# Kernel optimization log

Hardware: AMD Instinct MI355X
Metric: run time of the kernel (lower is better)

Reference implementation:

```python
import jax, jax.numpy as jnp
import numpy as np


def setup_inputs() -> dict:
    key = jax.random.key(0)
    k1, k2 = jax.random.split(key)
    B, N, D = 32, 8192, 128
    queries = jax.random.normal(k1, (B, 1, D), dtype=jnp.float32)
    values = jax.random.normal(k2, (B, N, D), dtype=jnp.float32)
    return {"queries": queries, "values": values}


def reference(queries, values):
    # scores: bmm(q [B,1,D], v^T [B,D,N]) -> [B,1,N] -> squeeze -> [B,N]
    scores = jnp.einsum("bqd,bnd->bn", queries, values)
    attn = jax.nn.softmax(scores, axis=-1)            # [B, N]
    # weighted sum over N; no explicit repeat needed (broadcast instead)
    context = jnp.einsum("bn,bnd->bd", attn, values)  # [B, D]
    return (attn, context)
```

## Files before the change

kernel.cpp:

```cpp
#include <hip/hip_runtime.h>
#include <hip/hip_bf16.h>
#include <math.h>

#define B 32
#define NROWS 8192
#define D 128
#define CHUNK 256
#define NCHUNK (NROWS / CHUNK)
#define RPW (CHUNK / 4)
#define NIT (RPW / 4)
#define SHIFT 16.0f

template <int CTRL>
__device__ __forceinline__ float dpp_add(float x) {
    int y = __builtin_amdgcn_update_dpp(
        0, __float_as_int(x), CTRL, 0xf, 0xf, true);
    return x + __int_as_float(y);
}

__device__ __forceinline__ void half_reduce(float p, float& s_lo, float& s_hi) {
    p = dpp_add<0x111>(p);
    p = dpp_add<0x112>(p);
    p = dpp_add<0x114>(p);
    p = dpp_add<0x118>(p);
    p = dpp_add<0x142>(p);
    s_lo = __int_as_float(__builtin_amdgcn_readlane(__float_as_int(p), 31));
    s_hi = __int_as_float(__builtin_amdgcn_readlane(__float_as_int(p), 63));
}

__global__ __launch_bounds__(256) void attend_k1(
    const float* __restrict__ q,
    const float* __restrict__ v,
    float* __restrict__ out_scores,
    float* __restrict__ part_l,
    float* __restrict__ part_o)
{
    __shared__ float s_sc[CHUNK];
    __shared__ float wl4[4];
    __shared__ float wo[4][D];

    const int b    = blockIdx.x >> 5;
    const int c    = blockIdx.x & (NCHUNK - 1);
    const int n0   = c * CHUNK;
    const int tid  = threadIdx.x;
    const int w    = tid >> 6;
    const int lane = tid & 63;
    const int half = lane >> 5;
    const int l32  = lane & 31;

    const float4 q4 = ((const float4*)(q + b * D))[l32];
    const float4* vb = (const float4*)(v + ((size_t)b * NROWS + n0 + w * RPW) * D);

    float l = 0.f;
    float4 acc = make_float4(0.f, 0.f, 0.f, 0.f);

    float4 a0 = vb[lane];
    float4 a1 = vb[64 + lane];

    #pragma unroll 2
    for (int i = 0; i < NIT; ++i) {
        const int j = (i + 1 < NIT) ? i + 1 : i;
        const float4 b0 = vb[j * 128 + lane];
        const float4 b1 = vb[j * 128 + 64 + lane];

        float p0 = a0.x * q4.x + a0.y * q4.y + a0.z * q4.z + a0.w * q4.w;
        float p1 = a1.x * q4.x + a1.y * q4.y + a1.z * q4.z + a1.w * q4.w;

        float s0lo, s0hi, s1lo, s1hi;
        half_reduce(p0, s0lo, s0hi);
        half_reduce(p1, s1lo, s1hi);
        const float s0 = half ? s0hi : s0lo;
        const float s1 = half ? s1hi : s1lo;
        if (l32 == 0) {
            s_sc[w * RPW + 4 * i + half]     = s0;
            s_sc[w * RPW + 4 * i + 2 + half] = s1;
        }

        const float e0 = __expf(s0 - SHIFT);
        const float e1 = __expf(s1 - SHIFT);
        l += e0 + e1;
        acc.x += e0 * a0.x + e1 * a1.x;
        acc.y += e0 * a0.y + e1 * a1.y;
        acc.z += e0 * a0.z + e1 * a1.z;
        acc.w += e0 * a0.w + e1 * a1.w;

        a0 = b0; a1 = b1;
    }

    l += __shfl_xor(l, 32, 64);
    acc.x += __shfl_xor(acc.x, 32, 64);
    acc.y += __shfl_xor(acc.y, 32, 64);
    acc.z += __shfl_xor(acc.z, 32, 64);
    acc.w += __shfl_xor(acc.w, 32, 64);
    if (half == 0) {
        ((float4*)wo[w])[l32] = acc;
        if (l32 == 0) wl4[w] = l;
    }
    __syncthreads();

    out_scores[(size_t)b * NROWS + n0 + tid] = s_sc[tid];

    if (tid < D) {
        const float o = wo[0][tid] + wo[1][tid] + wo[2][tid] + wo[3][tid];
        part_o[(size_t)blockIdx.x * D + tid] = o;
        if (tid == 0)
            part_l[blockIdx.x] = wl4[0] + wl4[1] + wl4[2] + wl4[3];
    }
}

__global__ __launch_bounds__(128) void attend_k2(
    const float* __restrict__ part_l,
    const float* __restrict__ part_o,
    float* __restrict__ out_ctx,
    float* __restrict__ bInvL)
{
    const int b = blockIdx.x;
    const int d = threadIdx.x;

    float L = 0.f, o = 0.f;
    #pragma unroll
    for (int c = 0; c < NCHUNK; ++c) {
        L += part_l[b * NCHUNK + c];
        o += part_o[(size_t)(b * NCHUNK + c) * D + d];
    }
    out_ctx[b * D + d] = o / L;
    if (d == 0) bInvL[b] = 1.0f / L;
}

__global__ __launch_bounds__(256) void attend_k3(
    float* __restrict__ attn,
    const float* __restrict__ bInvL)
{
    const int idx = blockIdx.x * 256 + threadIdx.x;
    const int b   = idx >> 11;
    const float invL = bInvL[b];
    float4 s = ((float4*)attn)[idx];
    s.x = __expf(s.x - SHIFT) * invL;
    s.y = __expf(s.y - SHIFT) * invL;
    s.z = __expf(s.z - SHIFT) * invL;
    s.w = __expf(s.w - SHIFT) * invL;
    ((float4*)attn)[idx] = s;
}

extern "C" void kernel_launch(void* const* d_in, const int* in_sizes, int n_in,
                              void* d_out, int out_size, void* d_ws, size_t ws_size,
                              hipStream_t stream) {
    const float* q = (const float*)d_in[0];
    const float* v = (const float*)d_in[1];
    float* out = (float*)d_out;

    float* ws      = (float*)d_ws;
    float* part_l  = ws;
    float* part_o  = part_l + B * NCHUNK;
    float* bInvL   = part_o + (size_t)B * NCHUNK * D;

    attend_k1<<<B * NCHUNK, 256, 0, stream>>>(q, v, out, part_l, part_o);
    attend_k2<<<B, 128, 0, stream>>>(part_l, part_o, out + (size_t)B * NROWS, bInvL);
    attend_k3<<<(B * NROWS / 4) / 256, 256, 0, stream>>>(out, bInvL);
}
```

Baseline: 194.5 us.

## Fuse reduction and normalization into main kernel via last-block atomic counter

Merges the three kernels into one: each chunk block increments a per-batch atomic counter, and the last block for a batch combines the partial sums, writes the context, and normalizes that batch's attention row in place. This removes two kernel launches and their gaps, plus the separate pass over the attention output. In exchange it adds a memset launch and fence/atomic overhead, and leaves the normalization tail on just 32 blocks (one per batch), each looping over 8192 elements.

Result: slower. 324.0 us (+66.6%).

```diff
diff --git a/kernel.cpp b/kernel.cpp
--- a/kernel.cpp
+++ b/kernel.cpp
@@ -28,16 +28,18 @@
     s_hi = __int_as_float(__builtin_amdgcn_readlane(__float_as_int(p), 63));
 }
 
-__global__ __launch_bounds__(256) void attend_k1(
+__global__ __launch_bounds__(256) void attend_fused(
     const float* __restrict__ q,
     const float* __restrict__ v,
-    float* __restrict__ out_scores,
+    float* __restrict__ out,
     float* __restrict__ part_l,
-    float* __restrict__ part_o)
+    float* __restrict__ part_o,
+    int*   __restrict__ counters)
 {
     __shared__ float s_sc[CHUNK];
     __shared__ float wl4[4];
     __shared__ float wo[4][D];
+    __shared__ int   sh_last;
 
     const int b    = blockIdx.x >> 5;
     const int c    = blockIdx.x & (NCHUNK - 1);
@@ -98,7 +100,7 @@
     }
     __syncthreads();
 
-    out_scores[(size_t)b * NROWS + n0 + tid] = s_sc[tid];
+    out[(size_t)b * NROWS + n0 + tid] = s_sc[tid];
 
     if (tid < D) {
         const float o = wo[0][tid] + wo[1][tid] + wo[2][tid] + wo[3][tid];
@@ -106,40 +108,40 @@
         if (tid == 0)
             part_l[blockIdx.x] = wl4[0] + wl4[1] + wl4[2] + wl4[3];
     }
-}
 
-__global__ __launch_bounds__(128) void attend_k2(
-    const float* __restrict__ part_l,
-    const float* __restrict__ part_o,
-    float* __restrict__ out_ctx,
-    float* __restrict__ bInvL)
-{
-    const int b = blockIdx.x;
-    const int d = threadIdx.x;
+    __threadfence();
+    __syncthreads();
+    if (tid == 0)
+        sh_last = (atomicAdd(&counters[b], 1) == NCHUNK - 1);
+    __syncthreads();
+    if (!sh_last) return;
 
-    float L = 0.f, o = 0.f;
+    __threadfence();
+
+    float L = 0.f;
     #pragma unroll
-    for (int c = 0; c < NCHUNK; ++c) {
-        L += part_l[b * NCHUNK + c];
-        o += part_o[(size_t)(b * NCHUNK + c) * D + d];
+    for (int cc = 0; cc < NCHUNK; ++cc)
+        L += part_l[b * NCHUNK + cc];
+    const float invL = 1.0f / L;
+
+    if (tid < D) {
+        float o = 0.f;
+        #pragma unroll
+        for (int cc = 0; cc < NCHUNK; ++cc)
+            o += part_o[(size_t)(b * NCHUNK + cc) * D + tid];
+        out[(size_t)B * NROWS + b * D + tid] = o * invL;
     }
-    out_ctx[b * D + d] = o / L;
-    if (d == 0) bInvL[b] = 1.0f / L;
-}
 
-__global__ __launch_bounds__(256) void attend_k3(
-    float* __restrict__ attn,
-    const float* __restrict__ bInvL)
-{
-    const int idx = blockIdx.x * 256 + threadIdx.x;
-    const int b   = idx >> 11;
-    const float invL = bInvL[b];
-    float4 s = ((float4*)attn)[idx];
-    s.x = __expf(s.x - SHIFT) * invL;
-    s.y = __expf(s.y - SHIFT) * invL;
-    s.z = __expf(s.z - SHIFT) * invL;
-    s.w = __expf(s.w - SHIFT) * invL;
-    ((float4*)attn)[idx] = s;
+    float4* attn4 = (float4*)(out + (size_t)b * NROWS);
+    #pragma unroll
+    for (int i = 0; i < (NROWS / 4) / 256; ++i) {
+        float4 s = attn4[i * 256 + tid];
+        s.x = __expf(s.x - SHIFT) * invL;
+        s.y = __expf(s.y - SHIFT) * invL;
+        s.z = __expf(s.z - SHIFT) * invL;
+        s.w = __expf(s.w - SHIFT) * invL;
+        attn4[i * 256 + tid] = s;
+    }
 }
 
 extern "C" void kernel_launch(void* const* d_in, const int* in_sizes, int n_in,
@@ -152,9 +154,8 @@
     float* ws      = (float*)d_ws;
     float* part_l  = ws;
     float* part_o  = part_l + B * NCHUNK;
-    float* bInvL   = part_o + (size_t)B * NCHUNK * D;
+    int*   counters = (int*)(part_o + (size_t)B * NCHUNK * D);
 
-    attend_k1<<<B * NCHUNK, 256, 0, stream>>>(q, v, out, part_l, part_o);
-    attend_k2<<<B, 128, 0, stream>>>(part_l, part_o, out + (size_t)B * NROWS, bInvL);
-    attend_k3<<<(B * NROWS / 4) / 256, 256, 0, stream>>>(out, bInvL);
+    hipMemsetAsync(counters, 0, B * sizeof(int), stream);
+    attend_fused<<<B * NCHUNK, 256, 0, stream>>>(q, v, out, part_l, part_o, counters);
 }
```
